# Performance work log

Measured on AMD Instinct MI355X. Metric: run time of the kernel, lower is better.

The kernel has to match this reference:

```python
import jax, jax.numpy as jnp
import numpy as np

B, N, C = 4, 2048, 768
H = 12
D = C // H  # head_dim = 64
SCALE = D ** -0.5


def setup_inputs() -> dict:
    key = jax.random.key(0)
    ks = jax.random.split(key, 9)
    x = jax.random.normal(ks[0], (B, N, C), dtype=jnp.float32)
    k_in = jax.random.normal(ks[1], (B, N, C), dtype=jnp.float32)
    v_in = jax.random.normal(ks[2], (B, N, C), dtype=jnp.float32)
    rel_pos_bias = jax.random.normal(ks[3], (H, N, N), dtype=jnp.float32)
    # learned params (nn.Linear stores weight [out, in]; y = x @ W.T + b)
    s = C ** -0.5
    Wq = jax.random.normal(ks[4], (C, C), dtype=jnp.float32) * s
    Wk = jax.random.normal(ks[5], (C, C), dtype=jnp.float32) * s
    Wv = jax.random.normal(ks[6], (C, C), dtype=jnp.float32) * s
    Wp = jax.random.normal(ks[7], (C, C), dtype=jnp.float32) * s
    bp = jax.random.normal(ks[8], (C,), dtype=jnp.float32) * 0.01
    return {"x": x, "k_in": k_in, "v_in": v_in, "rel_pos_bias": rel_pos_bias,
            "Wq": Wq, "Wk": Wk, "Wv": Wv, "Wp": Wp, "bp": bp}


def reference(x, k_in, v_in, rel_pos_bias, Wq, Wk, Wv, Wp, bp):
    # linear projections (no q/k/v bias since qkv_bias=False)
    q = jnp.einsum('bnc,dc->bnd', x, Wq)      # [B,N,C]
    k = jnp.einsum('bnc,dc->bnd', k_in, Wk)   # [B,Nk,C]
    v = jnp.einsum('bnc,dc->bnd', v_in, Wv)   # [B,Nv,C]
    # split heads -> [B,H,N,D]
    q = q.reshape(B, N, H, D).transpose(0, 2, 1, 3) * SCALE
    k = k.reshape(B, -1, H, D).transpose(0, 2, 1, 3)
    v = v.reshape(B, -1, H, D).transpose(0, 2, 1, 3)
    attn = jnp.einsum('bhnd,bhmd->bhnm', q, k)          # [B,H,N,Nk]
    attn = attn + rel_pos_bias[None]                    # additive rel-pos bias
    attn = jax.nn.softmax(attn, axis=-1)
    out = jnp.einsum('bhnm,bhmd->bhnd', attn, v)        # [B,H,N,D]
    out = out.transpose(0, 2, 1, 3).reshape(B, N, C)
    return jnp.einsum('bnc,dc->bnd', out, Wp) + bp
```

## Files before the change

kernel.cpp:

```cpp
#include <hip/hip_runtime.h>
#include <stdint.h>
#include <stddef.h>

#define B_ 4
#define N_ 2048
#define C_ 768
#define H_ 12
#define M_ (B_ * N_)

typedef __attribute__((ext_vector_type(8))) short bf16x8_t;
typedef __attribute__((ext_vector_type(4))) float f32x4_t;

__device__ __forceinline__ unsigned pack2_bf16(float f0, float f1) {
  unsigned u0 = __builtin_bit_cast(unsigned, f0) + 0x8000u;
  unsigned u1 = __builtin_bit_cast(unsigned, f1) + 0x8000u;
  return __builtin_amdgcn_perm(u1, u0, 0x07060302u);
}

__device__ __forceinline__ short f2bf(float f) {
  unsigned u = __builtin_bit_cast(unsigned, f);
  u = (u + 0x7FFFu + ((u >> 16) & 1u)) >> 16;
  return (short)u;
}
__device__ __forceinline__ short f2bf_fast(float f) {
  return (short)((__builtin_bit_cast(unsigned, f) + 0x8000u) >> 16);
}

__device__ __forceinline__ void gload_lds16(const short* g, const short* l) {
  __builtin_amdgcn_global_load_lds(
      (const __attribute__((address_space(1))) void*)g,
      (__attribute__((address_space(3))) void*)l, 16, 0, 0);
}

#define XV 1572864
#define WV 147456
__global__ __launch_bounds__(256) void cvt_all(
    const float* __restrict__ x, const float* __restrict__ kin, const float* __restrict__ vin,
    const float* __restrict__ wq, const float* __restrict__ wk, const float* __restrict__ wv,
    const float* __restrict__ wp,
    unsigned short* __restrict__ xb, unsigned short* __restrict__ kb, unsigned short* __restrict__ vb,
    unsigned short* __restrict__ wqb, unsigned short* __restrict__ wkb, unsigned short* __restrict__ wvb,
    unsigned short* __restrict__ wpb)
{
  int i = blockIdx.x * 256 + threadIdx.x;
  const float* s; unsigned short* d; int off;
  if      (i < XV)            { s = x;   d = xb;  off = i; }
  else if (i < 2 * XV)        { s = kin; d = kb;  off = i - XV; }
  else if (i < 3 * XV)        { s = vin; d = vb;  off = i - 2 * XV; }
  else if (i < 3 * XV + WV)   { s = wq;  d = wqb; off = i - 3 * XV; }
  else if (i < 3 * XV + 2*WV) { s = wk;  d = wkb; off = i - 3 * XV - WV; }
  else if (i < 3 * XV + 3*WV) { s = wv;  d = wvb; off = i - 3 * XV - 2 * WV; }
  else                        { s = wp;  d = wpb; off = i - 3 * XV - 3 * WV; }
  float4 v = ((const float4*)s)[off];
  uint2 p;
  p.x = pack2_bf16(v.x, v.y);
  p.y = pack2_bf16(v.z, v.w);
  ((uint2*)d)[off] = p;
}

__global__ __launch_bounds__(256) void proj_qkv(
    const short* __restrict__ xb, const short* __restrict__ kb, const short* __restrict__ vb,
    const short* __restrict__ wqb, const short* __restrict__ wkb, const short* __restrict__ wvb,
    short* __restrict__ q_ws, short* __restrict__ k_ws, short* __restrict__ vt_ws)
{
  const int z = blockIdx.z;
  const short* A = (z == 0) ? xb : (z == 1) ? kb : vb;
  const short* W = (z == 0) ? wqb : (z == 1) ? wkb : wvb;
  const int m0 = blockIdx.x * 128;
  const int n0 = blockIdx.y * 128;

  __shared__ short As[128 * 64];
  __shared__ short Bs[128 * 64];

  const int t = threadIdx.x;
  const int w = t >> 6, L = t & 63, L15 = L & 15, quad = L >> 4;
  const int wm = w & 1, wn = w >> 1;

  f32x4_t acc[4][4] = {};

  const short* ga = A + (size_t)(m0 + w * 32 + (L >> 3)) * C_ + (L & 7) * 8;
  const short* gb = W + (size_t)(n0 + w * 32 + (L >> 3)) * C_ + (L & 7) * 8;
  const short* la = &As[(w * 32) * 64];
  const short* lb = &Bs[(w * 32) * 64];

  for (int k0 = 0; k0 < C_; k0 += 64) {
    __syncthreads();
    #pragma unroll
    for (int i = 0; i < 4; ++i) {
      gload_lds16(ga + (size_t)i * 8 * C_ + k0, la + i * 512);
      gload_lds16(gb + (size_t)i * 8 * C_ + k0, lb + i * 512);
    }
    __syncthreads();
    #pragma unroll
    for (int kk = 0; kk < 2; ++kk) {
      bf16x8_t af[4], bf[4];
      #pragma unroll
      for (int mt = 0; mt < 4; ++mt)
        af[mt] = *(const bf16x8_t*)&As[(wm * 64 + mt * 16 + L15) * 64 + kk * 32 + quad * 8];
      #pragma unroll
      for (int nt = 0; nt < 4; ++nt)
        bf[nt] = *(const bf16x8_t*)&Bs[(wn * 64 + nt * 16 + L15) * 64 + kk * 32 + quad * 8];
      #pragma unroll
      for (int mt = 0; mt < 4; ++mt)
        #pragma unroll
        for (int nt = 0; nt < 4; ++nt)
          acc[mt][nt] = __builtin_amdgcn_mfma_f32_16x16x32_bf16(af[mt], bf[nt], acc[mt][nt], 0, 0, 0);
    }
  }

  short* outp = (z == 0) ? q_ws : (z == 1) ? k_ws : vt_ws;
  const float mul = (z == 0) ? 0.125f : 1.0f;
  #pragma unroll
  for (int mt = 0; mt < 4; ++mt) {
    const int m_base = m0 + wm * 64 + mt * 16 + quad * 4;
    #pragma unroll
    for (int nt = 0; nt < 4; ++nt) {
      const int c = n0 + wn * 64 + nt * 16 + L15;
      const int h = c >> 6, d = c & 63;
      #pragma unroll
      for (int r = 0; r < 4; ++r) {
        const int m = m_base + r;
        const int b = m >> 11, n = m & 2047;
        const float v = acc[mt][nt][r] * mul;
        size_t idx;
        if (z == 2) idx = ((size_t)(b * H_ + h) * 64 + d) * N_ + n;
        else        idx = ((size_t)(b * H_ + h) * N_ + n) * 64 + d;
        outp[idx] = f2bf(v);
      }
    }
  }
}

__global__ __launch_bounds__(256) void attn(
    const short* __restrict__ q_ws, const short* __restrict__ k_ws,
    const short* __restrict__ vt_ws, const float* __restrict__ rpb,
    short* __restrict__ attn_out)
{
  const int b = blockIdx.x & 3;
  const int m0 = (blockIdx.x >> 2) * 64;
  const int h = blockIdx.y;
  const int bh = b * H_ + h;

  __shared__ short Qs[64][72];
  __shared__ short Ks[64][72];
  __shared__ short Vts[80][72];
  __shared__ short Ps[4][16][72];

  const int t = threadIdx.x;
  const int w = t >> 6, L = t & 63, L15 = L & 15, quad = L >> 4;
  const int sr = t >> 2, sc = (t & 3) << 4;

  const short* qp  = q_ws  + ((size_t)bh * N_ + m0) * 64;
  const short* kp  = k_ws  + (size_t)bh * N_ * 64;
  const short* vtp = vt_ws + (size_t)bh * 64 * N_;
  const float* bpb = rpb + (size_t)h * N_ * N_;

  {
    const short* g = qp + t * 16;
    *(uint4*)&Qs[sr][sc]     = *(const uint4*)g;
    *(uint4*)&Qs[sr][sc + 8] = *(const uint4*)(g + 8);
  }
  for (int i = t; i < 16 * 72; i += 256) {
    const int rr = i / 72, cc = i % 72;
    Vts[64 + rr][cc] = (rr == 0) ? (short)0x3F80 : (short)0;
  }

  f32x4_t o[5] = {};

  for (int kv0 = 0; kv0 < N_; kv0 += 64) {
    __syncthreads();
    {
      const short* gk = kp + (size_t)kv0 * 64 + t * 16;
      *(uint4*)&Ks[sr][sc]     = *(const uint4*)gk;
      *(uint4*)&Ks[sr][sc + 8] = *(const uint4*)(gk + 8);
      const short* gv = vtp + (size_t)sr * N_ + kv0 + sc;
      *(uint4*)&Vts[sr][sc]     = *(const uint4*)gv;
      *(uint4*)&Vts[sr][sc + 8] = *(const uint4*)(gv + 8);
    }
    float bias[4][4];
    {
      const float* bq = bpb + (size_t)(m0 + w * 16 + quad * 4) * N_ + kv0 + L15;
      #pragma unroll
      for (int r = 0; r < 4; ++r)
        #pragma unroll
        for (int nt = 0; nt < 4; ++nt)
          bias[r][nt] = bq[(size_t)r * N_ + nt * 16];
    }
    __syncthreads();

    bf16x8_t a0 = *(const bf16x8_t*)&Qs[w * 16 + L15][quad * 8];
    bf16x8_t a1 = *(const bf16x8_t*)&Qs[w * 16 + L15][32 + quad * 8];
    f32x4_t s[4];
    #pragma unroll
    for (int nt = 0; nt < 4; ++nt) {
      f32x4_t sv = {bias[0][nt], bias[1][nt], bias[2][nt], bias[3][nt]};
      bf16x8_t b0 = *(const bf16x8_t*)&Ks[nt * 16 + L15][quad * 8];
      bf16x8_t b1 = *(const bf16x8_t*)&Ks[nt * 16 + L15][32 + quad * 8];
      sv = __builtin_amdgcn_mfma_f32_16x16x32_bf16(a0, b0, sv, 0, 0, 0);
      s[nt] = __builtin_amdgcn_mfma_f32_16x16x32_bf16(a1, b1, sv, 0, 0, 0);
    }

    #pragma unroll
    for (int nt = 0; nt < 4; ++nt)
      #pragma unroll
      for (int r = 0; r < 4; ++r)
        Ps[w][quad * 4 + r][nt * 16 + L15] = f2bf_fast(__expf(s[nt][r]));

    #pragma unroll
    for (int kk = 0; kk < 2; ++kk) {
      bf16x8_t pa = *(const bf16x8_t*)&Ps[w][L15][kk * 32 + quad * 8];
      #pragma unroll
      for (int nt = 0; nt < 5; ++nt) {
        bf16x8_t vb = *(const bf16x8_t*)&Vts[nt * 16 + L15][kk * 32 + quad * 8];
        o[nt] = __builtin_amdgcn_mfma_f32_16x16x32_bf16(pa, vb, o[nt], 0, 0, 0);
      }
    }
  }

  float rl[4];
  #pragma unroll
  for (int r = 0; r < 4; ++r) {
    const float l = __shfl(o[4][r], quad * 16);
    rl[r] = 1.0f / l;
  }
  const int n_base = m0 + w * 16 + quad * 4;
  #pragma unroll
  for (int nt = 0; nt < 4; ++nt) {
    #pragma unroll
    for (int r = 0; r < 4; ++r) {
      const float v = o[nt][r] * rl[r];
      attn_out[((size_t)(b * N_ + n_base + r)) * C_ + h * 64 + nt * 16 + L15] = f2bf(v);
    }
  }
}

__global__ __launch_bounds__(256) void proj_out(
    const short* __restrict__ Abf, const short* __restrict__ wpb,
    const float* __restrict__ bpv, float* __restrict__ out)
{
  const int m0 = blockIdx.x * 128;
  const int n0 = blockIdx.y * 128;

  __shared__ short As[128 * 64];
  __shared__ short Bs[128 * 64];

  const int t = threadIdx.x;
  const int w = t >> 6, L = t & 63, L15 = L & 15, quad = L >> 4;
  const int wm = w & 1, wn = w >> 1;

  f32x4_t acc[4][4] = {};

  const short* ga = Abf + (size_t)(m0 + w * 32 + (L >> 3)) * C_ + (L & 7) * 8;
  const short* gb = wpb + (size_t)(n0 + w * 32 + (L >> 3)) * C_ + (L & 7) * 8;
  const short* la = &As[(w * 32) * 64];
  const short* lb = &Bs[(w * 32) * 64];

  for (int k0 = 0; k0 < C_; k0 += 64) {
    __syncthreads();
    #pragma unroll
    for (int i = 0; i < 4; ++i) {
      gload_lds16(ga + (size_t)i * 8 * C_ + k0, la + i * 512);
      gload_lds16(gb + (size_t)i * 8 * C_ + k0, lb + i * 512);
    }
    __syncthreads();
    #pragma unroll
    for (int kk = 0; kk < 2; ++kk) {
      bf16x8_t af[4], bf[4];
      #pragma unroll
      for (int mt = 0; mt < 4; ++mt)
        af[mt] = *(const bf16x8_t*)&As[(wm * 64 + mt * 16 + L15) * 64 + kk * 32 + quad * 8];
      #pragma unroll
      for (int nt = 0; nt < 4; ++nt)
        bf[nt] = *(const bf16x8_t*)&Bs[(wn * 64 + nt * 16 + L15) * 64 + kk * 32 + quad * 8];
      #pragma unroll
      for (int mt = 0; mt < 4; ++mt)
        #pragma unroll
        for (int nt = 0; nt < 4; ++nt)
          acc[mt][nt] = __builtin_amdgcn_mfma_f32_16x16x32_bf16(af[mt], bf[nt], acc[mt][nt], 0, 0, 0);
    }
  }

  #pragma unroll
  for (int mt = 0; mt < 4; ++mt) {
    const int m_base = m0 + wm * 64 + mt * 16 + quad * 4;
    #pragma unroll
    for (int nt = 0; nt < 4; ++nt) {
      const int c = n0 + wn * 64 + nt * 16 + L15;
      const float bb = bpv[c];
      #pragma unroll
      for (int r = 0; r < 4; ++r)
        out[(size_t)(m_base + r) * C_ + c] = acc[mt][nt][r] + bb;
    }
  }
}

extern "C" void kernel_launch(void* const* d_in, const int* in_sizes, int n_in,
                              void* d_out, int out_size, void* d_ws, size_t ws_size,
                              hipStream_t stream) {
  const float* x    = (const float*)d_in[0];
  const float* k_in = (const float*)d_in[1];
  const float* v_in = (const float*)d_in[2];
  const float* rpb  = (const float*)d_in[3];
  const float* Wq   = (const float*)d_in[4];
  const float* Wk   = (const float*)d_in[5];
  const float* Wv   = (const float*)d_in[6];
  const float* Wp   = (const float*)d_in[7];
  const float* bp   = (const float*)d_in[8];
  float* out = (float*)d_out;

  const size_t SZ = (size_t)B_ * H_ * N_ * 64 * sizeof(short);
  const size_t WSZ = (size_t)C_ * C_ * sizeof(short);
  char* ws = (char*)d_ws;
  short* q_ws  = (short*)(ws);
  short* k_ws  = (short*)(ws + SZ);
  short* vt_ws = (short*)(ws + 2 * SZ);
  short* ao_ws = (short*)(ws + 3 * SZ);
  short* xb    = (short*)(ws + 4 * SZ);
  short* kb    = (short*)(ws + 5 * SZ);
  short* vb    = (short*)(ws + 6 * SZ);
  short* wqb   = (short*)(ws + 7 * SZ);
  short* wkb   = (short*)(ws + 7 * SZ + WSZ);
  short* wvb   = (short*)(ws + 7 * SZ + 2 * WSZ);
  short* wpb   = (short*)(ws + 7 * SZ + 3 * WSZ);

  cvt_all<<<(3 * XV + 4 * WV + 255) / 256, 256, 0, stream>>>(
      x, k_in, v_in, Wq, Wk, Wv, Wp,
      (unsigned short*)xb, (unsigned short*)kb, (unsigned short*)vb,
      (unsigned short*)wqb, (unsigned short*)wkb, (unsigned short*)wvb, (unsigned short*)wpb);
  proj_qkv<<<dim3(M_ / 128, C_ / 128, 3), 256, 0, stream>>>(
      xb, kb, vb, wqb, wkb, wvb, q_ws, k_ws, vt_ws);
  attn<<<dim3(B_ * (N_ / 64), H_), 256, 0, stream>>>(q_ws, k_ws, vt_ws, rpb, ao_ws);
  proj_out<<<dim3(M_ / 128, C_ / 128), 256, 0, stream>>>(ao_ws, wpb, bp, out);
}
```

Before: 512.9 us.

## Retile attention to 128 query rows, swizzle LDS, stage V-transpose through LDS

The attention kernel now handles 128 query rows per block, 32 per wave. Q fragments stay in registers, and LDS tiles for K, V and P use an XOR swizzle in place of padding. The row sum is accumulated in registers with shuffles, replacing the extra ones-column MFMA. The grid is flattened and remapped so blocks sharing a head land on the same XCD, and launch bounds request 3 blocks per SM. The V projection epilogue transposes through shared memory so it can write coalesced 16-byte stores, at the cost of extra syncs and more register pressure.

```diff
diff --git a/kernel.cpp b/kernel.cpp
--- a/kernel.cpp
+++ b/kernel.cpp
@@ -69,8 +69,9 @@
   const int m0 = blockIdx.x * 128;
   const int n0 = blockIdx.y * 128;
 
-  __shared__ short As[128 * 64];
-  __shared__ short Bs[128 * 64];
+  __shared__ __align__(16) short smem[128 * 136];
+  short* As = smem;
+  short* Bs = smem + 128 * 64;
 
   const int t = threadIdx.x;
   const int w = t >> 6, L = t & 63, L15 = L & 15, quad = L >> 4;
@@ -80,8 +81,8 @@
 
   const short* ga = A + (size_t)(m0 + w * 32 + (L >> 3)) * C_ + (L & 7) * 8;
   const short* gb = W + (size_t)(n0 + w * 32 + (L >> 3)) * C_ + (L & 7) * 8;
-  const short* la = &As[(w * 32) * 64];
-  const short* lb = &Bs[(w * 32) * 64];
+  const short* la = As + (w * 32) * 64;
+  const short* lb = Bs + (w * 32) * 64;
 
   for (int k0 = 0; k0 < C_; k0 += 64) {
     __syncthreads();
@@ -108,129 +109,188 @@
     }
   }
 
-  short* outp = (z == 0) ? q_ws : (z == 1) ? k_ws : vt_ws;
-  const float mul = (z == 0) ? 0.125f : 1.0f;
-  #pragma unroll
-  for (int mt = 0; mt < 4; ++mt) {
-    const int m_base = m0 + wm * 64 + mt * 16 + quad * 4;
-    #pragma unroll
-    for (int nt = 0; nt < 4; ++nt) {
-      const int c = n0 + wn * 64 + nt * 16 + L15;
-      const int h = c >> 6, d = c & 63;
-      #pragma unroll
-      for (int r = 0; r < 4; ++r) {
-        const int m = m_base + r;
-        const int b = m >> 11, n = m & 2047;
-        const float v = acc[mt][nt][r] * mul;
-        size_t idx;
-        if (z == 2) idx = ((size_t)(b * H_ + h) * 64 + d) * N_ + n;
-        else        idx = ((size_t)(b * H_ + h) * N_ + n) * 64 + d;
-        outp[idx] = f2bf(v);
-      }
-    }
-  }
-}
-
-__global__ __launch_bounds__(256) void attn(
+  if (z != 2) {
+    short* outp = (z == 0) ? q_ws : k_ws;
+    const float mul = (z == 0) ? 0.125f : 1.0f;
+    #pragma unroll
+    for (int mt = 0; mt < 4; ++mt) {
+      const int m_base = m0 + wm * 64 + mt * 16 + quad * 4;
+      #pragma unroll
+      for (int nt = 0; nt < 4; ++nt) {
+        const int c = n0 + wn * 64 + nt * 16 + L15;
+        const int h = c >> 6, d = c & 63;
+        #pragma unroll
+        for (int r = 0; r < 4; ++r) {
+          const int m = m_base + r;
+          const int b = m >> 11, n = m & 2047;
+          outp[((size_t)(b * H_ + h) * N_ + n) * 64 + d] = f2bf(acc[mt][nt][r] * mul);
+        }
+      }
+    }
+  } else {
+    __syncthreads();
+    #pragma unroll
+    for (int mt = 0; mt < 4; ++mt) {
+      const int ml = wm * 64 + mt * 16 + quad * 4;
+      #pragma unroll
+      for (int nt = 0; nt < 4; ++nt) {
+        const int cl = wn * 64 + nt * 16 + L15;
+        #pragma unroll
+        for (int r = 0; r < 4; ++r)
+          smem[cl * 136 + ml + r] = f2bf(acc[mt][nt][r]);
+      }
+    }
+    __syncthreads();
+    const int bb = m0 >> 11;
+    const int nn0 = m0 & 2047;
+    #pragma unroll
+    for (int pp = 0; pp < 8; ++pp) {
+      const int cl = pp * 16 + (t >> 4);
+      const int mg = t & 15;
+      const uint4 val = *(const uint4*)&smem[cl * 136 + mg * 8];
+      const int cg = n0 + cl;
+      *(uint4*)&vt_ws[(((size_t)(bb * H_ + (cg >> 6))) * 64 + (cg & 63)) * N_ + nn0 + mg * 8] = val;
+    }
+  }
+}
+
+__global__ __launch_bounds__(256, 3) void attn(
     const short* __restrict__ q_ws, const short* __restrict__ k_ws,
     const short* __restrict__ vt_ws, const float* __restrict__ rpb,
     short* __restrict__ attn_out)
 {
-  const int b = blockIdx.x & 3;
-  const int m0 = (blockIdx.x >> 2) * 64;
-  const int h = blockIdx.y;
+  const int p  = blockIdx.x;
+  const int lw = (p & 7) * 96 + (p >> 3);
+  const int h  = lw >> 6;
+  const int xl = lw & 63;
+  const int b  = xl & 3;
+  const int m0 = (xl >> 2) * 128;
   const int bh = b * H_ + h;
 
-  __shared__ short Qs[64][72];
-  __shared__ short Ks[64][72];
-  __shared__ short Vts[80][72];
-  __shared__ short Ps[4][16][72];
+  __shared__ __align__(16) short Ks [64 * 64];
+  __shared__ __align__(16) short Vts[64 * 64];
+  __shared__ __align__(16) short Ps [4][32 * 64];
 
   const int t = threadIdx.x;
   const int w = t >> 6, L = t & 63, L15 = L & 15, quad = L >> 4;
-  const int sr = t >> 2, sc = (t & 3) << 4;
+  const int sr  = t >> 2;
+  const int scb = (t & 3) << 5;
+  const int swz_w = (sr & 7) << 4;
 
   const short* qp  = q_ws  + ((size_t)bh * N_ + m0) * 64;
   const short* kp  = k_ws  + (size_t)bh * N_ * 64;
   const short* vtp = vt_ws + (size_t)bh * 64 * N_;
   const float* bpb = rpb + (size_t)h * N_ * N_;
 
-  {
-    const short* g = qp + t * 16;
-    *(uint4*)&Qs[sr][sc]     = *(const uint4*)g;
-    *(uint4*)&Qs[sr][sc + 8] = *(const uint4*)(g + 8);
-  }
-  for (int i = t; i < 16 * 72; i += 256) {
-    const int rr = i / 72, cc = i % 72;
-    Vts[64 + rr][cc] = (rr == 0) ? (short)0x3F80 : (short)0;
-  }
-
-  f32x4_t o[5] = {};
+  bf16x8_t aq[2][2];
+  #pragma unroll
+  for (int mt = 0; mt < 2; ++mt)
+    #pragma unroll
+    for (int kk = 0; kk < 2; ++kk)
+      aq[mt][kk] = *(const bf16x8_t*)(qp + (size_t)(w * 32 + mt * 16 + L15) * 64 + kk * 32 + quad * 8);
+
+  f32x4_t o[2][4] = {};
+  float psum[2][4] = {};
 
   for (int kv0 = 0; kv0 < N_; kv0 += 64) {
     __syncthreads();
     {
-      const short* gk = kp + (size_t)kv0 * 64 + t * 16;
-      *(uint4*)&Ks[sr][sc]     = *(const uint4*)gk;
-      *(uint4*)&Ks[sr][sc + 8] = *(const uint4*)(gk + 8);
-      const short* gv = vtp + (size_t)sr * N_ + kv0 + sc;
-      *(uint4*)&Vts[sr][sc]     = *(const uint4*)gv;
-      *(uint4*)&Vts[sr][sc + 8] = *(const uint4*)(gv + 8);
-    }
-    float bias[4][4];
+      const short* gk = kp + (size_t)(kv0 + sr) * 64 + (scb >> 1);
+      const uint4 k0 = *(const uint4*)gk;
+      const uint4 k1 = *(const uint4*)(gk + 8);
+      const short* gv = vtp + (size_t)sr * N_ + kv0 + (scb >> 1);
+      const uint4 v0 = *(const uint4*)gv;
+      const uint4 v1 = *(const uint4*)(gv + 8);
+      *(uint4*)((char*)Ks  + sr * 128 + (scb ^ swz_w))        = k0;
+      *(uint4*)((char*)Ks  + sr * 128 + ((scb + 16) ^ swz_w)) = k1;
+      *(uint4*)((char*)Vts + sr * 128 + (scb ^ swz_w))        = v0;
+      *(uint4*)((char*)Vts + sr * 128 + ((scb + 16) ^ swz_w)) = v1;
+    }
+    float bias[2][4][4];
     {
-      const float* bq = bpb + (size_t)(m0 + w * 16 + quad * 4) * N_ + kv0 + L15;
-      #pragma unroll
-      for (int r = 0; r < 4; ++r)
-        #pragma unroll
-        for (int nt = 0; nt < 4; ++nt)
-          bias[r][nt] = bq[(size_t)r * N_ + nt * 16];
-    }
-    __syncthreads();
-
-    bf16x8_t a0 = *(const bf16x8_t*)&Qs[w * 16 + L15][quad * 8];
-    bf16x8_t a1 = *(const bf16x8_t*)&Qs[w * 16 + L15][32 + quad * 8];
-    f32x4_t s[4];
+      const float* bq = bpb + (size_t)(m0 + w * 32 + quad * 4) * N_ + kv0 + L15;
+      #pragma unroll
+      for (int mt = 0; mt < 2; ++mt)
+        #pragma unroll
+        for (int r = 0; r < 4; ++r)
+          #pragma unroll
+          for (int nt = 0; nt < 4; ++nt)
+            bias[mt][nt][r] = bq[(size_t)(mt * 16 + r) * N_ + nt * 16];
+    }
+    __syncthreads();
+
+    f32x4_t s[2][4];
     #pragma unroll
     for (int nt = 0; nt < 4; ++nt) {
-      f32x4_t sv = {bias[0][nt], bias[1][nt], bias[2][nt], bias[3][nt]};
-      bf16x8_t b0 = *(const bf16x8_t*)&Ks[nt * 16 + L15][quad * 8];
-      bf16x8_t b1 = *(const bf16x8_t*)&Ks[nt * 16 + L15][32 + quad * 8];
-      sv = __builtin_amdgcn_mfma_f32_16x16x32_bf16(a0, b0, sv, 0, 0, 0);
-      s[nt] = __builtin_amdgcn_mfma_f32_16x16x32_bf16(a1, b1, sv, 0, 0, 0);
-    }
-
+      const int row = nt * 16 + L15;
+      const char* kbp = (const char*)Ks + row * 128;
+      const int sx = (row & 7) << 4;
+      const bf16x8_t b0 = *(const bf16x8_t*)(kbp + ((quad * 16) ^ sx));
+      const bf16x8_t b1 = *(const bf16x8_t*)(kbp + ((64 + quad * 16) ^ sx));
+      #pragma unroll
+      for (int mt = 0; mt < 2; ++mt) {
+        f32x4_t sv = {bias[mt][nt][0], bias[mt][nt][1], bias[mt][nt][2], bias[mt][nt][3]};
+        sv = __builtin_amdgcn_mfma_f32_16x16x32_bf16(aq[mt][0], b0, sv, 0, 0, 0);
+        s[mt][nt] = __builtin_amdgcn_mfma_f32_16x16x32_bf16(aq[mt][1], b1, sv, 0, 0, 0);
+      }
+    }
+
+    #pragma unroll
+    for (int mt = 0; mt < 2; ++mt)
+      #pragma unroll
+      for (int nt = 0; nt < 4; ++nt)
+        #pragma unroll
+        for (int r = 0; r < 4; ++r) {
+          const float e = __expf(s[mt][nt][r]);
+          psum[mt][r] += e;
+          const int qrow = mt * 16 + quad * 4 + r;
+          const int cb = (nt * 32 + L15 * 2) ^ ((qrow & 7) << 4);
+          *(short*)((char*)Ps[w] + qrow * 128 + cb) = f2bf_fast(e);
+        }
+
+    #pragma unroll
+    for (int kk = 0; kk < 2; ++kk) {
+      bf16x8_t pa[2];
+      #pragma unroll
+      for (int mt = 0; mt < 2; ++mt) {
+        const int row = mt * 16 + L15;
+        pa[mt] = *(const bf16x8_t*)((char*)Ps[w] + row * 128 +
+                                    ((kk * 64 + quad * 16) ^ ((row & 7) << 4)));
+      }
+      #pragma unroll
+      for (int nt = 0; nt < 4; ++nt) {
+        const int row = nt * 16 + L15;
+        const bf16x8_t vbf = *(const bf16x8_t*)((char*)Vts + row * 128 +
+                                                ((kk * 64 + quad * 16) ^ ((row & 7) << 4)));
+        #pragma unroll
+        for (int mt = 0; mt < 2; ++mt)
+          o[mt][nt] = __builtin_amdgcn_mfma_f32_16x16x32_bf16(pa[mt], vbf, o[mt][nt], 0, 0, 0);
+      }
+    }
+  }
+
+  #pragma unroll
+  for (int mt = 0; mt < 2; ++mt)
+    #pragma unroll
+    for (int r = 0; r < 4; ++r) {
+      float v = psum[mt][r];
+      v += __shfl_xor(v, 1);
+      v += __shfl_xor(v, 2);
+      v += __shfl_xor(v, 4);
+      v += __shfl_xor(v, 8);
+      psum[mt][r] = 1.0f / v;
+    }
+
+  #pragma unroll
+  for (int mt = 0; mt < 2; ++mt) {
+    const int n_base = m0 + w * 32 + mt * 16 + quad * 4;
     #pragma unroll
     for (int nt = 0; nt < 4; ++nt)
       #pragma unroll
-      for (int r = 0; r < 4; ++r)
-        Ps[w][quad * 4 + r][nt * 16 + L15] = f2bf_fast(__expf(s[nt][r]));
-
-    #pragma unroll
-    for (int kk = 0; kk < 2; ++kk) {
-      bf16x8_t pa = *(const bf16x8_t*)&Ps[w][L15][kk * 32 + quad * 8];
-      #pragma unroll
-      for (int nt = 0; nt < 5; ++nt) {
-        bf16x8_t vb = *(const bf16x8_t*)&Vts[nt * 16 + L15][kk * 32 + quad * 8];
-        o[nt] = __builtin_amdgcn_mfma_f32_16x16x32_bf16(pa, vb, o[nt], 0, 0, 0);
-      }
-    }
-  }
-
-  float rl[4];
-  #pragma unroll
-  for (int r = 0; r < 4; ++r) {
-    const float l = __shfl(o[4][r], quad * 16);
-    rl[r] = 1.0f / l;
-  }
-  const int n_base = m0 + w * 16 + quad * 4;
-  #pragma unroll
-  for (int nt = 0; nt < 4; ++nt) {
-    #pragma unroll
-    for (int r = 0; r < 4; ++r) {
-      const float v = o[nt][r] * rl[r];
-      attn_out[((size_t)(b * N_ + n_base + r)) * C_ + h * 64 + nt * 16 + L15] = f2bf(v);
-    }
+      for (int r = 0; r < 4; ++r) {
+        const float v = o[mt][nt][r] * psum[mt][r];
+        attn_out[((size_t)(b * N_ + n_base + r)) * C_ + h * 64 + nt * 16 + L15] = f2bf(v);
+      }
   }
 }
 
@@ -329,6 +389,6 @@
       (unsigned short*)wqb, (unsigned short*)wkb, (unsigned short*)wvb, (unsigned short*)wpb);
   proj_qkv<<<dim3(M_ / 128, C_ / 128, 3), 256, 0, stream>>>(
       xb, kb, vb, wqb, wkb, wvb, q_ws, k_ws, vt_ws);
-  attn<<<dim3(B_ * (N_ / 64), H_), 256, 0, stream>>>(q_ws, k_ws, vt_ws, rpb, ao_ws);
+  attn<<<dim3(B_ * (N_ / 128) * H_), 256, 0, stream>>>(q_ws, k_ws, vt_ws, rpb, ao_ws);
   proj_out<<<dim3(M_ / 128, C_ / 128), 256, 0, stream>>>(ao_ws, wpb, bp, out);
 }
```

New measurement: 473.0 us. -7.8%, faster.
